# Kernel tuning notes

Measured on AMD Instinct MI355X. Metric: run time of the kernel, lower is better.

## Reference

```python
import jax, jax.numpy as jnp
import numpy as np

NUM_CLASSES = 30522


def setup_inputs() -> dict:
    key = jax.random.key(0)
    k1, k2 = jax.random.split(key)
    B, S = 1024, 256
    input_ids = jax.random.randint(k1, (B, S), 0, NUM_CLASSES)  # token ids
    weights = jax.random.uniform(k2, (B, S, 1), dtype=jnp.float32)  # per-token weights
    return {"input_ids": input_ids, "weights": weights}


def reference(input_ids, weights):
    # Torch: one_hot(ids, V) * weights -> (B,S,V), max over dim=1 -> (B,V), cast bf16.
    # Equivalent (without the huge (B,S,V) intermediate): scatter-max of the
    # per-token weight into its vocab slot, with a 0 baseline everywhere
    # (non-matching one-hot entries contribute 0 to the max).
    B, S = input_ids.shape
    w = weights[..., 0]  # (B, S)
    base = jnp.zeros((B, NUM_CLASSES), dtype=weights.dtype)
    b_idx = jnp.arange(B)[:, None]  # (B, 1) broadcasts against (B, S) ids
    out = base.at[b_idx, input_ids].max(w)  # (B, V) scatter-max
    return out.astype(jnp.bfloat16)
```

## Files before the change

kernel.cpp:

```cpp
#include <hip/hip_runtime.h>

#define VOCAB 30522
#define SEQ   256

extern "C" __global__ __launch_bounds__(256)
void TargetEncoder_532575944857_kernel(const int* __restrict__ ids,
                                       const float* __restrict__ ws,
                                       unsigned int* __restrict__ out,
                                       int n_tok) {
    const int t = blockIdx.x * blockDim.x + threadIdx.x;
    if (t >= n_tok) return;

    const int   id = ids[t];
    const float w  = ws[t];
    if ((unsigned)id >= (unsigned)VOCAB) return;

    const unsigned u   = __float_as_uint(w);
    const unsigned val = ((u + 0x7FFFu + ((u >> 16) & 1u)) >> 16) << 16;
    if (val == 0u) return;

    const int b = t >> 8;
    atomicMax(out + ((long long)b * VOCAB + id), val);
}

extern "C" void kernel_launch(void* const* d_in, const int* in_sizes, int n_in,
                              void* d_out, int out_size, void* d_ws, size_t ws_size,
                              hipStream_t stream) {
    const int*   ids = (const int*)d_in[0];
    const float* ws  = (const float*)d_in[1];
    const int n_tok  = in_sizes[0];

    (void)hipMemsetAsync(d_out, 0, (size_t)out_size * sizeof(float), stream);

    TargetEncoder_532575944857_kernel<<<(n_tok + 255) / 256, 256, 0, stream>>>(
        ids, ws, (unsigned int*)d_out, n_tok);
}
```

Baseline: 136.7 us.

## Fuse output zeroing into scatter-max kernel with per-block row ownership

```diff
diff --git a/kernel.cpp b/kernel.cpp
--- a/kernel.cpp
+++ b/kernel.cpp
@@ -1,26 +1,38 @@
 #include <hip/hip_runtime.h>
 
-#define VOCAB 30522
-#define SEQ   256
+#define BATCH     1024
+#define SEQ       256
+#define VOCAB     30522
+#define ROWS_PER_BLOCK 2
+#define THREADS   512
+#define BLK_U4    15261
 
-extern "C" __global__ __launch_bounds__(256)
+extern "C" __global__ __launch_bounds__(THREADS)
 void TargetEncoder_532575944857_kernel(const int* __restrict__ ids,
                                        const float* __restrict__ ws,
-                                       unsigned int* __restrict__ out,
-                                       int n_tok) {
-    const int t = blockIdx.x * blockDim.x + threadIdx.x;
-    if (t >= n_tok) return;
+                                       unsigned int* __restrict__ out) {
+    const int blk = blockIdx.x;
+    const int t   = threadIdx.x;
 
-    const int   id = ids[t];
-    const float w  = ws[t];
-    if ((unsigned)id >= (unsigned)VOCAB) return;
+    const int tok = blk * (ROWS_PER_BLOCK * SEQ) + t;
+    const int   id = ids[tok];
+    const float w  = ws[tok];
 
-    const unsigned u   = __float_as_uint(w);
-    const unsigned val = ((u + 0x7FFFu + ((u >> 16) & 1u)) >> 16) << 16;
-    if (val == 0u) return;
+    uint4* zbase = (uint4*)(out + (long long)blk * (ROWS_PER_BLOCK * VOCAB));
+    const uint4 z = make_uint4(0u, 0u, 0u, 0u);
+    #pragma unroll 4
+    for (int i = t; i < BLK_U4; i += THREADS) zbase[i] = z;
 
-    const int b = t >> 8;
-    atomicMax(out + ((long long)b * VOCAB + id), val);
+    __syncthreads();
+
+    if ((unsigned)id < (unsigned)VOCAB) {
+        const unsigned u   = __float_as_uint(w);
+        const unsigned val = ((u + 0x7FFFu + ((u >> 16) & 1u)) >> 16) << 16;
+        if (val != 0u) {
+            const int row = blk * ROWS_PER_BLOCK + (t >> 8);
+            atomicMax(out + ((long long)row * VOCAB + id), val);
+        }
+    }
 }
 
 extern "C" void kernel_launch(void* const* d_in, const int* in_sizes, int n_in,
@@ -28,10 +40,8 @@
                               hipStream_t stream) {
     const int*   ids = (const int*)d_in[0];
     const float* ws  = (const float*)d_in[1];
-    const int n_tok  = in_sizes[0];
 
-    (void)hipMemsetAsync(d_out, 0, (size_t)out_size * sizeof(float), stream);
-
-    TargetEncoder_532575944857_kernel<<<(n_tok + 255) / 256, 256, 0, stream>>>(
-        ids, ws, (unsigned int*)d_out, n_tok);
+    TargetEncoder_532575944857_kernel
+        <<<BATCH / ROWS_PER_BLOCK, THREADS, 0, stream>>>(
+            ids, ws, (unsigned int*)d_out);
 }
```

Result: no change. 137.7 us (+0.8%).
